# Kernel tuning notes

Measured on AMD Instinct MI355X. Metric: run time of the kernel, lower is better.

Reference implementation:

```python
import jax, jax.numpy as jnp
import numpy as np

D_MODEL = 512
D_STATE = 16
D_INNER = 2 * D_MODEL  # expand_factor=2
IN_CH = 256
B_SZ, H_SZ, W_SZ = 4, 32, 32


def setup_inputs() -> dict:
    key = jax.random.key(0)
    ks = jax.random.split(key, 24)
    f = jax.random.normal
    inp = {}
    inp["x_V"] = f(ks[0], (B_SZ, IN_CH, H_SZ, W_SZ), jnp.float32)
    inp["x_I"] = f(ks[1], (B_SZ, IN_CH, H_SZ, W_SZ), jnp.float32)
    # channel_reduce: 1x1 conv + BN (inference stats)
    inp["conv_red_w"] = f(ks[2], (D_MODEL, IN_CH), jnp.float32) * 0.05
    inp["bn_red_g"] = jnp.ones((D_MODEL,), jnp.float32)
    inp["bn_red_b"] = jnp.zeros((D_MODEL,), jnp.float32)
    inp["bn_red_m"] = jnp.zeros((D_MODEL,), jnp.float32)
    inp["bn_red_v"] = jnp.ones((D_MODEL,), jnp.float32)
    # channel_restore: 1x1 conv + BN
    inp["conv_res_w"] = f(ks[3], (IN_CH, D_MODEL), jnp.float32) * 0.05
    inp["bn_res_g"] = jnp.ones((IN_CH,), jnp.float32)
    inp["bn_res_b"] = jnp.zeros((IN_CH,), jnp.float32)
    inp["bn_res_m"] = jnp.zeros((IN_CH,), jnp.float32)
    inp["bn_res_v"] = jnp.ones((IN_CH,), jnp.float32)
    # lambda_predictor convs (1x1 on pooled features == linear)
    inp["lam_w1"] = f(ks[4], (D_MODEL // 4, D_MODEL * 2), jnp.float32) * 0.05
    inp["lam_b1"] = jnp.zeros((D_MODEL // 4,), jnp.float32)
    inp["lam_w2"] = f(ks[5], (2, D_MODEL // 4), jnp.float32) * 0.05
    inp["lam_b2"] = jnp.zeros((2,), jnp.float32)
    # two SimplifiedMamba2Blocks
    for i, p in enumerate(["V", "I"]):
        kk = jax.random.split(ks[6 + i], 6)
        inp[p + "_in_w"] = f(kk[0], (2 * D_INNER, D_MODEL), jnp.float32) * 0.03
        inp[p + "_out_w"] = f(kk[1], (D_MODEL, D_INNER), jnp.float32) * 0.03
        # A = -exp(A_log) in (-1, -0.05): stable decay
        inp[p + "_A_log"] = jnp.log(jax.random.uniform(kk[2], (D_INNER, D_STATE), jnp.float32, 0.05, 0.95))
        inp[p + "_B"] = f(kk[3], (D_INNER, D_STATE), jnp.float32) * 0.05
        inp[p + "_C"] = jnp.full((D_INNER, D_STATE), 0.01, jnp.float32)
        inp[p + "_ln_g"] = jnp.ones((D_MODEL,), jnp.float32)
        inp[p + "_ln_b"] = jnp.zeros((D_MODEL,), jnp.float32)
    inp["gate"] = jnp.asarray(0.1, jnp.float32)
    return inp


def _bn(x, g, b, m, v):
    # x: (B,C,H,W); inference-mode batchnorm
    return (x - m[:, None, None]) / jnp.sqrt(v[:, None, None] + 1e-5) * g[:, None, None] + b[:, None, None]


def _conv1x1(x, w):
    return jnp.einsum('bchw,oc->bohw', x, w)


def _ssm_scan(x_ssm, A, Bm, Cm, reverse):
    # x_ssm: (B,L,I); A,Bm,Cm: (I,S)
    bsz = x_ssm.shape[0]
    h0 = jnp.zeros((bsz, A.shape[0], A.shape[1]), x_ssm.dtype)

    def step(h, xt):  # xt: (B,I)
        h = jnp.clip(h * A + xt[:, :, None] * Bm, -10.0, 10.0)
        return h, jnp.einsum('bis,is->bi', h, Cm)

    _, ys = jax.lax.scan(step, h0, jnp.swapaxes(x_ssm, 0, 1), reverse=reverse)
    return jnp.swapaxes(ys, 0, 1)  # (B,L,I), in original time order


def _mamba(x, ln_g, ln_b, in_w, out_w, A_log, Bm, Cm):
    # LayerNorm
    mu = jnp.mean(x, -1, keepdims=True)
    var = jnp.mean((x - mu) ** 2, -1, keepdims=True)
    xn = (x - mu) / jnp.sqrt(var + 1e-5) * ln_g + ln_b
    xp = xn @ in_w.T  # (B,L,2*I)
    x_ssm, gate = jnp.split(xp, 2, axis=-1)
    A = jnp.clip(-jnp.exp(A_log), -10.0, -0.01)
    yf = _ssm_scan(x_ssm, A, Bm, Cm, False)
    yb = _ssm_scan(x_ssm, A, Bm, Cm, True)
    out = 0.5 * (yf + yb) * jax.nn.silu(gate)
    return out @ out_w.T


def reference(x_V, x_I, conv_red_w, bn_red_g, bn_red_b, bn_red_m, bn_red_v,
              conv_res_w, bn_res_g, bn_res_b, bn_res_m, bn_res_v,
              lam_w1, lam_b1, lam_w2, lam_b2,
              V_in_w, V_out_w, V_A_log, V_B, V_C, V_ln_g, V_ln_b,
              I_in_w, I_out_w, I_A_log, I_B, I_C, I_ln_g, I_ln_b, gate):
    B, _, H, W = x_V.shape
    xVr = jax.nn.relu(_bn(_conv1x1(x_V, conv_red_w), bn_red_g, bn_red_b, bn_red_m, bn_red_v))
    xIr = jax.nn.relu(_bn(_conv1x1(x_I, conv_red_w), bn_red_g, bn_red_b, bn_red_m, bn_red_v))
    # same spatial size -> adaptive pooling and [:B] slicing are identities
    conc = jnp.concatenate([xVr, xIr], axis=1)  # (B, 2*d_model, H, W)

    def lam(c):
        p = jnp.mean(c, axis=(2, 3))  # global avg pool -> (B, 2*d_model)
        h1 = jax.nn.relu(p @ lam_w1.T + lam_b1)
        return jax.nn.softmax(h1 @ lam_w2.T + lam_b2, axis=-1)  # (B,2)

    lamV = lam(conc)
    lamI = lam(conc)

    seq_V = jnp.swapaxes(xVr.reshape(B, D_MODEL, H * W), 1, 2)  # (B,L,D)
    seq_I = jnp.swapaxes(xIr.reshape(B, D_MODEL, H * W), 1, 2)

    outV_std = _mamba(seq_V, V_ln_g, V_ln_b, V_in_w, V_out_w, V_A_log, V_B, V_C)
    outI_std = _mamba(seq_I, I_ln_g, I_ln_b, I_in_w, I_out_w, I_A_log, I_B, I_C)
    outV_cross = _mamba(seq_V, V_ln_g, V_ln_b, V_in_w, V_out_w, V_A_log, jax.lax.stop_gradient(I_B), V_C)
    outI_cross = _mamba(seq_I, I_ln_g, I_ln_b, I_in_w, I_out_w, I_A_log, jax.lax.stop_gradient(V_B), I_C)

    outV = lamV[:, 0][:, None, None] * outV_std + lamV[:, 1][:, None, None] * outV_cross
    outI = lamI[:, 0][:, None, None] * outI_std + lamI[:, 1][:, None, None] * outI_cross

    featV = jnp.swapaxes(outV, 1, 2).reshape(B, D_MODEL, H, W)
    featI = jnp.swapaxes(outI, 1, 2).reshape(B, D_MODEL, H, W)
    featV = _bn(_conv1x1(featV, conv_res_w), bn_res_g, bn_res_b, bn_res_m, bn_res_v)
    featI = _bn(_conv1x1(featI, conv_res_w), bn_res_g, bn_res_b, bn_res_m, bn_res_v)

    g = jax.nn.sigmoid(gate)
    return (x_V + g * featV, x_I + g * featI)
```

## Files before the change

kernel.cpp:

```cpp
#include <hip/hip_runtime.h>
#include <hip/hip_bf16.h>
#include <math.h>

#define L_SZ 1024
#define DM   512
#define DI   1024
#define NS   16
#define CH   256

typedef float4 f4;
typedef __attribute__((ext_vector_type(8))) short short8;
typedef __attribute__((ext_vector_type(8))) unsigned short u16x8;
typedef __attribute__((ext_vector_type(4))) float f32x4;

__device__ __forceinline__ float bf2f(ushort u) {
    union { unsigned int i; float f; } x; x.i = ((unsigned int)u) << 16; return x.f;
}
__device__ __forceinline__ ushort f2bf(float f) {
    union { float f; unsigned int i; } x; x.f = f;
    unsigned int r = x.i + 0x7FFFu + ((x.i >> 16) & 1u);
    return (ushort)(r >> 16);
}
__device__ __forceinline__ uint pkbf(float a, float b) {
    union { __hip_bfloat162 h; uint u; } c;
    c.h = __float22bfloat162_rn(make_float2(a, b));
    return c.u;
}

#define GLOAD16(gp, lp) \
  __builtin_amdgcn_global_load_lds((const __attribute__((address_space(1))) void*)(gp), \
                                   (__attribute__((address_space(3))) void*)(lp), 16, 0, 0)

__global__ __launch_bounds__(256) void k_prep(
    const float* __restrict__ s0, const float* __restrict__ s1,
    const float* __restrict__ s2, const float* __restrict__ s3,
    const float* __restrict__ s4, const float* __restrict__ s5,
    ushort* __restrict__ d0, ushort* __restrict__ d1,
    ushort* __restrict__ d2, ushort* __restrict__ d3,
    ushort* __restrict__ d4, ushort* __restrict__ d5,
    const float* __restrict__ xv, const float* __restrict__ xi,
    ushort* __restrict__ xtv, ushort* __restrict__ xti,
    float* __restrict__ p, unsigned int* __restrict__ cnt)
{
    __shared__ float tile[32][36];
    const int bid = blockIdx.x;
    const int t = threadIdx.x;
    if (bid < 2304) {
        const float* s; ushort* d; int rel;
        if      (bid < 128)  { s = s0; d = d0; rel = bid; }
        else if (bid < 256)  { s = s1; d = d1; rel = bid - 128; }
        else if (bid < 1280) { s = s2; d = d2; rel = bid - 256; }
        else                 { s = s3; d = d3; rel = bid - 1280; }
        const int i = rel * 256 + t;
        f4 v = ((const f4*)s)[i];
        ushort4 o;
        o.x = f2bf(v.x); o.y = f2bf(v.y); o.z = f2bf(v.z); o.w = f2bf(v.w);
        ((ushort4*)d)[i] = o;
        return;
    }
    if (bid < 3328) {
        const int rel = (bid < 2816) ? bid - 2304 : bid - 2816;
        const float* wo = (bid < 2816) ? s4 : s5;
        ushort* wt      = (bid < 2816) ? d4 : d5;
        const int kt = rel & 31, dt = rel >> 5;
        const int d0_ = dt * 32, k0 = kt * 32;
        {
            int cc = t >> 3, ll4 = (t & 7) << 2;
            f4 v = *(const f4*)(wo + (size_t)(d0_ + cc) * 1024 + k0 + ll4);
            tile[cc][ll4 + 0] = v.x; tile[cc][ll4 + 1] = v.y;
            tile[cc][ll4 + 2] = v.z; tile[cc][ll4 + 3] = v.w;
        }
        __syncthreads();
        {
            int ll = t >> 3, cc4 = (t & 7) << 2;
            ushort4 o;
            o.x = f2bf(tile[cc4 + 0][ll]); o.y = f2bf(tile[cc4 + 1][ll]);
            o.z = f2bf(tile[cc4 + 2][ll]); o.w = f2bf(tile[cc4 + 3][ll]);
            *(ushort4*)(wt + (size_t)(k0 + ll) * 512 + d0_ + cc4) = o;
        }
        return;
    }
    if (bid < 5376) {
        const int rel = bid - 3328;
        const int l0 = (rel & 31) * 32, c0 = ((rel >> 5) & 7) * 32;
        const int z = rel >> 8;
        const int b = z & 3, st = z >> 2;
        const float* x = st ? xi : xv;
        ushort* xt = st ? xti : xtv;
        {
            int cc = t >> 3, ll4 = (t & 7) << 2;
            f4 v = *(const f4*)(x + ((size_t)(b * CH + c0 + cc)) * L_SZ + l0 + ll4);
            tile[cc][ll4 + 0] = v.x; tile[cc][ll4 + 1] = v.y;
            tile[cc][ll4 + 2] = v.z; tile[cc][ll4 + 3] = v.w;
        }
        __syncthreads();
        {
            int ll = t >> 3, cc4 = (t & 7) << 2;
            ushort4 o;
            o.x = f2bf(tile[cc4 + 0][ll]); o.y = f2bf(tile[cc4 + 1][ll]);
            o.z = f2bf(tile[cc4 + 2][ll]); o.w = f2bf(tile[cc4 + 3][ll]);
            *(ushort4*)(xt + ((size_t)(b * L_SZ + l0 + ll)) * CH + c0 + cc4) = o;
        }
        return;
    }
    const f4 z4 = {0.f, 0.f, 0.f, 0.f};
    ((f4*)p)[t]       = z4;
    ((f4*)p)[t + 256] = z4;
    ((f4*)p)[t + 512] = z4;
    ((f4*)p)[t + 768] = z4;
    if (t == 0) *cnt = 0u;
}

template<int MODE, int BM, int BN, int OS>
__global__ __launch_bounds__(256) void k_gemm(
    const ushort* __restrict__ A0, const ushort* __restrict__ A1,
    const ushort* __restrict__ B0, const ushort* __restrict__ B1,
    int K,
    float* __restrict__ o0, float* __restrict__ o1,
    ushort* __restrict__ ob0, ushort* __restrict__ ob1,
    ushort* __restrict__ sb0, ushort* __restrict__ sb1,
    const float* __restrict__ pg, const float* __restrict__ pb,
    const float* __restrict__ pm, const float* __restrict__ pv,
    const float* __restrict__ x0, const float* __restrict__ x1,
    const float* __restrict__ gate, float* __restrict__ pp)
{
    constexpr int MT   = BM / 32;
    constexpr int NT   = BN / 32;
    constexpr int ASEG = BM / 16;
    constexpr int NSEG = (BM + BN) / 16;
    constexpr int SPW  = NSEG / 4;
    __shared__ __align__(16) ushort Sl[2][(BM + BN) * 32];
    const int t = threadIdx.x;
    const int wv = t >> 6, lane = t & 63;
    const int n0 = blockIdx.x * BN, m0 = blockIdx.y * BM;
    const int st = blockIdx.z;
    const ushort* Ap = st ? A1 : A0;
    const ushort* Bp = st ? B1 : B0;
    const int wm = wv >> 1, wn = wv & 1;
    const int lrow = lane & 15, q = lane >> 4;
    f32x4 acc[MT][NT];
    #pragma unroll
    for (int a_ = 0; a_ < MT; ++a_)
        #pragma unroll
        for (int b_ = 0; b_ < NT; ++b_)
            acc[a_][b_] = (f32x4){0.f, 0.f, 0.f, 0.f};
    const int srow = lane >> 2;
    const int skk  = (((lane & 3) ^ ((lane >> 3) & 3)) << 3);
    const int koff = ((q ^ ((lrow >> 1) & 3)) << 3);
    #pragma unroll
    for (int s2 = 0; s2 < SPW; ++s2) {
        const int seg = wv * SPW + s2;
        const int grow = (seg < ASEG) ? (m0 + seg * 16 + srow)
                                      : (n0 + (seg - ASEG) * 16 + srow);
        const ushort* src = (seg < ASEG) ? Ap : Bp;
        GLOAD16(src + (size_t)grow * K + skk, &Sl[0][seg * 512]);
    }
    int cur = 0;
    for (int k0 = 0; k0 < K; k0 += 32) {
        if (k0 + 32 < K) {
            #pragma unroll
            for (int s2 = 0; s2 < SPW; ++s2) {
                const int seg = wv * SPW + s2;
                const int grow = (seg < ASEG) ? (m0 + seg * 16 + srow)
                                              : (n0 + (seg - ASEG) * 16 + srow);
                const ushort* src = (seg < ASEG) ? Ap : Bp;
                GLOAD16(src + (size_t)grow * K + (k0 + 32) + skk, &Sl[cur ^ 1][seg * 512]);
            }
            if constexpr (SPW == 2)      asm volatile("s_waitcnt vmcnt(2)" ::: "memory");
            else if constexpr (SPW == 3) asm volatile("s_waitcnt vmcnt(3)" ::: "memory");
            else                         asm volatile("s_waitcnt vmcnt(4)" ::: "memory");
        } else {
            asm volatile("s_waitcnt vmcnt(0)" ::: "memory");
        }
        __builtin_amdgcn_s_barrier();
        short8 af[MT], bfr[NT];
        #pragma unroll
        for (int mt = 0; mt < MT; ++mt)
            af[mt] = *(const short8*)&Sl[cur][(wm * (MT * 16) + mt * 16 + lrow) * 32 + koff];
        #pragma unroll
        for (int nt = 0; nt < NT; ++nt)
            bfr[nt] = *(const short8*)&Sl[cur][(BM + wn * (NT * 16) + nt * 16 + lrow) * 32 + koff];
        #pragma unroll
        for (int mt = 0; mt < MT; ++mt)
            #pragma unroll
            for (int nt = 0; nt < NT; ++nt) {
                if constexpr (MODE == 1)
                    acc[mt][nt] = __builtin_amdgcn_mfma_f32_16x16x32_bf16(bfr[nt], af[mt], acc[mt][nt], 0, 0, 0);
                else
                    acc[mt][nt] = __builtin_amdgcn_mfma_f32_16x16x32_bf16(af[mt], bfr[nt], acc[mt][nt], 0, 0, 0);
            }
        asm volatile("s_waitcnt lgkmcnt(0)" ::: "memory");
        __builtin_amdgcn_sched_barrier(0);
        __builtin_amdgcn_s_barrier();
        cur ^= 1;
    }
    if (MODE == 0) {
        ushort* sq = st ? ob1 : ob0;
        const int b = m0 >> 10;
        #pragma unroll
        for (int nt = 0; nt < NT; ++nt) {
            const int gn = n0 + wn * (NT * 16) + nt * 16 + lrow;
            const float s  = pg[gn] * rsqrtf(pv[gn] + 1e-5f);
            const float sh = pb[gn] - pm[gn] * s;
            float psum = 0.f;
            #pragma unroll
            for (int mt = 0; mt < MT; ++mt) {
                const int gm = m0 + wm * (MT * 16) + mt * 16 + q * 4;
                float v[4];
                #pragma unroll
                for (int r = 0; r < 4; ++r) {
                    v[r] = fmaxf(fmaf(acc[mt][nt][r], s, sh), 0.f);
                    psum += v[r];
                }
                const uint u01 = pkbf(v[0], v[1]);
                const uint u23 = pkbf(v[2], v[3]);
                ushort* bp = sq + (size_t)gm * DM + gn;
                bp[0]      = (ushort)u01;
                bp[DM]     = (ushort)(u01 >> 16);
                bp[2 * DM] = (ushort)u23;
                bp[3 * DM] = (ushort)(u23 >> 16);
            }
            psum += __shfl_xor(psum, 16, 64);
            psum += __shfl_xor(psum, 32, 64);
            if (q == 0)
                atomicAdd(pp + (b * 1024 + st * 512 + gn), psum * (1.0f / 1024.0f));
        }
    } else if (MODE == 1) {
        const bool isx = (n0 < 1024);
        ushort* xp = st ? ob1 : ob0;
        ushort* sp = st ? sb1 : sb0;
        #pragma unroll
        for (int mt = 0; mt < MT; ++mt) {
            const int gm = m0 + wm * (MT * 16) + mt * 16 + lrow;
            #pragma unroll
            for (int nt = 0; nt < NT; ++nt) {
                const int gnb = n0 + wn * (NT * 16) + nt * 16 + q * 4;
                if (isx) {
                    const uint u01 = pkbf(acc[mt][nt][0], acc[mt][nt][1]);
                    const uint u23 = pkbf(acc[mt][nt][2], acc[mt][nt][3]);
                    *(uint2*)(xp + (size_t)gm * DI + gnb) = make_uint2(u01, u23);
                } else {
                    float sv[4];
                    #pragma unroll
                    for (int r = 0; r < 4; ++r) {
                        const float v = acc[mt][nt][r];
                        sv[r] = v / (1.f + __expf(-v));
                    }
                    const uint u01 = pkbf(sv[0], sv[1]);
                    const uint u23 = pkbf(sv[2], sv[3]);
                    *(uint2*)(sp + (size_t)gm * DI + gnb - 1024) = make_uint2(u01, u23);
                }
            }
        }
    } else if (MODE == 2) {
        ushort* fp_ = st ? ob1 : ob0;
        #pragma unroll
        for (int nt = 0; nt < NT; ++nt) {
            const int gn = n0 + wn * (NT * 16) + nt * 16 + lrow;
            #pragma unroll
            for (int mt = 0; mt < MT; ++mt) {
                const int gm = m0 + wm * (MT * 16) + mt * 16 + q * 4;
                const uint u01 = pkbf(acc[mt][nt][0], acc[mt][nt][1]);
                const uint u23 = pkbf(acc[mt][nt][2], acc[mt][nt][3]);
                ushort* bp = fp_ + (size_t)gm * OS + gn;
                bp[0]      = (ushort)u01;
                bp[OS]     = (ushort)(u01 >> 16);
                bp[2 * OS] = (ushort)u23;
                bp[3 * OS] = (ushort)(u23 >> 16);
            }
        }
    } else {
        const float* xin = st ? x1 : x0;
        float* op = st ? o1 : o0;
        const float g = 1.f / (1.f + __expf(-gate[0]));
        #pragma unroll
        for (int nt = 0; nt < NT; ++nt) {
            const int gn = n0 + wn * (NT * 16) + nt * 16 + lrow;
            const float s  = pg[gn] * rsqrtf(pv[gn] + 1e-5f);
            const float sh = pb[gn] - pm[gn] * s;
            #pragma unroll
            for (int mt = 0; mt < MT; ++mt) {
                const int gmb = m0 + wm * (MT * 16) + mt * 16 + q * 4;
                const int b = gmb >> 10, l = gmb & 1023;
                const size_t off = ((size_t)(b * CH + gn)) * L_SZ + l;
                f4 xi = *(const f4*)(xin + off);
                f4 o;
                o.x = xi.x + g * fmaf(acc[mt][nt][0], s, sh);
                o.y = xi.y + g * fmaf(acc[mt][nt][1], s, sh);
                o.z = xi.z + g * fmaf(acc[mt][nt][2], s, sh);
                o.w = xi.w + g * fmaf(acc[mt][nt][3], s, sh);
                *(f4*)(op + off) = o;
            }
        }
    }
}

__global__ __launch_bounds__(256) void k_lnlam(
    const ushort* __restrict__ seq0, const ushort* __restrict__ seq1,
    const float* __restrict__ g0, const float* __restrict__ b0,
    const float* __restrict__ g1, const float* __restrict__ b1,
    ushort* __restrict__ ln0, ushort* __restrict__ ln1,
    const float* __restrict__ p, const float* __restrict__ w1,
    const float* __restrict__ lb1, const float* __restrict__ w2,
    const float* __restrict__ lb2, float* __restrict__ h1,
    float* __restrict__ lamo, unsigned int* __restrict__ cnt)
{
    const int t = threadIdx.x, lane = t & 63, wv = t >> 6;
    if (blockIdx.x >= 1024) {
        __shared__ float lsm[8];
        __shared__ unsigned int tick;
        const int lbk = (blockIdx.x - 1024) * 2 + blockIdx.y;
        const int idx = lbk * 4 + wv;
        const int b = idx >> 7, j = idx & 127;
        const float* pb = p + b * 1024;
        const float* wr = w1 + j * 1024;
        float s = 0.f;
        #pragma unroll
        for (int k = 0; k < 16; ++k)
            s = fmaf(pb[lane + k * 64], wr[lane + k * 64], s);
        #pragma unroll
        for (int off = 1; off < 64; off <<= 1) s += __shfl_xor(s, off, 64);
        if (lane == 0) h1[idx] = fmaxf(s + lb1[j], 0.f);
        __threadfence();
        __syncthreads();
        if (t == 0) tick = atomicAdd(cnt, 1u);
        __syncthreads();
        if (tick != 127u) return;
        __threadfence();
        {
            const int g32 = t >> 5, l32 = t & 31;
            const int bb = g32 >> 1, kk = g32 & 1;
            const float* hb = h1 + bb * 128;
            const float* wr2 = w2 + kk * 128;
            float ss = 0.f;
            #pragma unroll
            for (int u = 0; u < 4; ++u)
                ss = fmaf(hb[l32 + u * 32], wr2[l32 + u * 32], ss);
            #pragma unroll
            for (int off = 1; off < 32; off <<= 1) ss += __shfl_xor(ss, off, 64);
            if (l32 == 0) lsm[g32] = ss + lb2[kk];
        }
        __syncthreads();
        if (t < 4) {
            const float a0 = lsm[t * 2], a1 = lsm[t * 2 + 1];
            const float m  = fmaxf(a0, a1);
            const float e0 = __expf(a0 - m), e1 = __expf(a1 - m);
            const float inv = 1.f / (e0 + e1);
            lamo[t * 2 + 0] = e0 * inv;
            lamo[t * 2 + 1] = e1 * inv;
        }
        return;
    }
    const int row = blockIdx.x * 4 + wv, st = blockIdx.y;
    const ushort* seq = st ? seq1 : seq0;
    const float* gg  = st ? g1 : g0;
    const float* bb  = st ? b1 : b0;
    ushort* ln = st ? ln1 : ln0;
    const u16x8 v = *(const u16x8*)(seq + (size_t)row * DM + lane * 8);
    float f[8];
    float s = 0.f, ss = 0.f;
    #pragma unroll
    for (int i = 0; i < 8; ++i) {
        f[i] = bf2f(v[i]);
        s += f[i];
        ss = fmaf(f[i], f[i], ss);
    }
    #pragma unroll
    for (int off = 1; off < 64; off <<= 1) {
        s += __shfl_xor(s, off, 64); ss += __shfl_xor(ss, off, 64);
    }
    const float mu = s * (1.f / 512.f);
    const float rstd = rsqrtf(ss * (1.f / 512.f) - mu * mu + 1e-5f);
    const f4 gv0 = *(const f4*)(gg + lane * 8);
    const f4 gv1 = *(const f4*)(gg + lane * 8 + 4);
    const f4 bv0 = *(const f4*)(bb + lane * 8);
    const f4 bv1 = *(const f4*)(bb + lane * 8 + 4);
    const float gvv[8] = {gv0.x, gv0.y, gv0.z, gv0.w, gv1.x, gv1.y, gv1.z, gv1.w};
    const float bvv[8] = {bv0.x, bv0.y, bv0.z, bv0.w, bv1.x, bv1.y, bv1.z, bv1.w};
    u16x8 o;
    #pragma unroll
    for (int i = 0; i < 8; i += 2) {
        const uint u = pkbf(fmaf((f[i]     - mu) * rstd, gvv[i],     bvv[i]),
                            fmaf((f[i + 1] - mu) * rstd, gvv[i + 1], bvv[i + 1]));
        o[i]     = (ushort)u;
        o[i + 1] = (ushort)(u >> 16);
    }
    *(u16x8*)(ln + (size_t)row * DM + lane * 8) = o;
}

__global__ __launch_bounds__(128, 2) void k_scan(
    const ushort* __restrict__ xsV, const ushort* __restrict__ xsI,
    const ushort* __restrict__ sgV, const ushort* __restrict__ sgI,
    const float* __restrict__ VA, const float* __restrict__ VB,
    const float* __restrict__ VC, const float* __restrict__ IA,
    const float* __restrict__ IB, const float* __restrict__ IC,
    const float* __restrict__ lam,
    ushort* __restrict__ yV, ushort* __restrict__ yI)
{
    __shared__ __align__(16) ushort xt[256][64];
    const int t = threadIdx.x;
    const int dir = t & 1;
    const int il = t >> 1;
    const int b = blockIdx.y;
    const int st = blockIdx.z >> 3, j = blockIdx.z & 7;
    const int c0 = blockIdx.x * 64;
    const ushort* xrow  = (st ? xsI : xsV) + (size_t)b * L_SZ * DI + c0;
    const ushort* sgrow = (st ? sgI : sgV) + (size_t)b * L_SZ * DI + c0;
    ushort* yrow        = (st ? yI  : yV ) + (size_t)b * L_SZ * DI + c0;
    const float* Alog = st ? IA : VA;
    const float* Cm   = st ? IC : VC;
    const float* Bown = st ? IB : VB;
    const float* Both = st ? VB : IB;
    const float lam0 = lam[b * 2 + 0], lam1 = lam[b * 2 + 1];
    const int row0 = j << 7;
    const int srow = t >> 3;
    const int scol = (t & 7) << 3;
    #pragma unroll
    for (int i = 0; i < 16; ++i) {
        int r = row0 - 64 + i * 16 + srow;
        r = max(0, min(1023, r));
        GLOAD16(xrow + (size_t)r * DI + scol, &xt[i * 16 + srow][0]);
    }
    float a[16], w[16], g[16];
    {
        const int cb = (c0 + il) * NS;
        #pragma unroll
        for (int s4 = 0; s4 < 4; ++s4) {
            const f4 av = *(const f4*)(Alog + cb + s4 * 4);
            const f4 cv = *(const f4*)(Cm   + cb + s4 * 4);
            const f4 bo = *(const f4*)(Bown + cb + s4 * 4);
            const f4 bt = *(const f4*)(Both + cb + s4 * 4);
            const float avv[4] = {av.x, av.y, av.z, av.w};
            const float cvv[4] = {cv.x, cv.y, cv.z, cv.w};
            const float bov[4] = {bo.x, bo.y, bo.z, bo.w};
            const float btv[4] = {bt.x, bt.y, bt.z, bt.w};
            #pragma unroll
            for (int q = 0; q < 4; ++q) {
                const int s = s4 * 4 + q;
                a[s] = fminf(fmaxf(-__expf(avv[q]), -10.f), -0.01f);
                w[s] = 0.5f * cvv[q] * fmaf(lam0, bov[q], lam1 * btv[q]);
                g[s] = 0.f;
            }
        }
    }
    __syncthreads();

    const ushort* xtf = &xt[0][0];
    int toff = (dir ? 255 : 0) * 64 + il;
    const int tstep = dir ? -64 : 64;

    float vp0, vp1, vp2, vp3;

#define XPRE(V) { V = bf2f(xtf[toff]); toff += tstep; }
#define UPD(V) { _Pragma("unroll") \
    for (int s = 0; s < 16; ++s) g[s] = fmaf(a[s], g[s], V); }
#define YROW(V, Y) { float ye_ = 0.f, yo_ = 0.f; \
    _Pragma("unroll") \
    for (int s = 0; s < 8; ++s) { \
        g[s]     = fmaf(a[s],     g[s],     V); ye_ = fmaf(g[s],     w[s],     ye_); \
        g[s + 8] = fmaf(a[s + 8], g[s + 8], V); yo_ = fmaf(g[s + 8], w[s + 8], yo_); \
    } \
    Y = ye_ + yo_; }

    XPRE(vp0) XPRE(vp1) XPRE(vp2) XPRE(vp3)
    #pragma unroll
    for (int k = 0; k < 16; ++k) {
        UPD(vp0) XPRE(vp0) UPD(vp1) XPRE(vp1)
        UPD(vp2) XPRE(vp2) UPD(vp3) XPRE(vp3)
    }
    if ((j == 0 && dir == 0) || (j == 7 && dir == 1)) {
        #pragma unroll
        for (int s = 0; s < 16; ++s) g[s] = 0.f;
    }

#define SP4(WA, WB) { float y0_, y1_, y2_, y3_; \
    YROW(vp0, y0_) XPRE(vp0) YROW(vp1, y1_) XPRE(vp1) \
    YROW(vp2, y2_) XPRE(vp2) YROW(vp3, y3_) XPRE(vp3) \
    WA = (uint)f2bf(y0_) | ((uint)f2bf(y1_) << 16); \
    WB = (uint)f2bf(y2_) | ((uint)f2bf(y3_) << 16); }

#define SGPRE(K, S0, S1, S2, S3) { \
    S0 = bf2f(sgrow[(size_t)(row0 + (dir ? (63 - 2*(K))     : (64 + 2*(K))))     * DI + il]); \
    S1 = bf2f(sgrow[(size_t)(row0 + (dir ? (62 - 2*(K))     : (65 + 2*(K))))     * DI + il]); \
    S2 = bf2f(sgrow[(size_t)(row0 + (dir ? (61 - 2*(K))     : (66 + 2*(K))))     * DI + il]); \
    S3 = bf2f(sgrow[(size_t)(row0 + (dir ? (60 - 2*(K))     : (67 + 2*(K))))     * DI + il]); }

#define F4(K, W1, W2, S0, S1, S2, S3) { \
    const uint p1_ = __shfl_xor(W1, 1, 64); \
    float y_; \
    YROW(vp0, y_) XPRE(vp0) \
    { const int r_ = row0 + (dir ? (63 - 2*(K)) : (64 + 2*(K))); \
      yrow[(size_t)r_ * DI + il] = f2bf((y_ + bf2f((ushort)(p1_ >> 16))) * S0); } \
    YROW(vp1, y_) XPRE(vp1) \
    { const int r_ = row0 + (dir ? (62 - 2*(K)) : (65 + 2*(K))); \
      yrow[(size_t)r_ * DI + il] = f2bf((y_ + bf2f((ushort)(p1_ & 0xFFFFu))) * S1); } \
    const uint p2_ = __shfl_xor(W2, 1, 64); \
    YROW(vp2, y_) XPRE(vp2) \
    { const int r_ = row0 + (dir ? (61 - 2*(K)) : (66 + 2*(K))); \
      yrow[(size_t)r_ * DI + il] = f2bf((y_ + bf2f((ushort)(p2_ >> 16))) * S2); } \
    YROW(vp3, y_) XPRE(vp3) \
    { const int r_ = row0 + (dir ? (60 - 2*(K)) : (67 + 2*(K))); \
      yrow[(size_t)r_ * DI + il] = f2bf((y_ + bf2f((ushort)(p2_ & 0xFFFFu))) * S3); } }

    uint s00, s01, s02, s03, s04, s05, s06, s07;
    uint s08, s09, s10, s11, s12, s13, s14, s15;
    uint s16, s17, s18, s19, s20, s21, s22, s23;
    uint s24, s25, s26, s27, s28, s29, s30, s31;

    SP4(s00, s01) SP4(s02, s03) SP4(s04, s05) SP4(s06, s07)
    SP4(s08, s09) SP4(s10, s11) SP4(s12, s13) SP4(s14, s15)
    SP4(s16, s17) SP4(s18, s19) SP4(s20, s21) SP4(s22, s23)
    SP4(s24, s25) SP4(s26, s27) SP4(s28, s29) SP4(s30, s31)

    float sa0, sa1, sa2, sa3, sb0, sb1, sb2, sb3;
    SGPRE(0,  sa0, sa1, sa2, sa3)
    SGPRE(2,  sb0, sb1, sb2, sb3)
    F4(0,  s31, s30, sa0, sa1, sa2, sa3) SGPRE(4,  sa0, sa1, sa2, sa3)
    F4(2,  s29, s28, sb0, sb1, sb2, sb3) SGPRE(6,  sb0, sb1, sb2, sb3)
    F4(4,  s27, s26, sa0, sa1, sa2, sa3) SGPRE(8,  sa0, sa1, sa2, sa3)
    F4(6,  s25, s24, sb0, sb1, sb2, sb3) SGPRE(10, sb0, sb1, sb2, sb3)
    F4(8,  s23, s22, sa0, sa1, sa2, sa3) SGPRE(12, sa0, sa1, sa2, sa3)
    F4(10, s21, s20, sb0, sb1, sb2, sb3) SGPRE(14, sb0, sb1, sb2, sb3)
    F4(12, s19, s18, sa0, sa1, sa2, sa3) SGPRE(16, sa0, sa1, sa2, sa3)
    F4(14, s17, s16, sb0, sb1, sb2, sb3) SGPRE(18, sb0, sb1, sb2, sb3)
    F4(16, s15, s14, sa0, sa1, sa2, sa3) SGPRE(20, sa0, sa1, sa2, sa3)
    F4(18, s13, s12, sb0, sb1, sb2, sb3) SGPRE(22, sb0, sb1, sb2, sb3)
    F4(20, s11, s10, sa0, sa1, sa2, sa3) SGPRE(24, sa0, sa1, sa2, sa3)
    F4(22, s09, s08, sb0, sb1, sb2, sb3) SGPRE(26, sb0, sb1, sb2, sb3)
    F4(24, s07, s06, sa0, sa1, sa2, sa3) SGPRE(28, sa0, sa1, sa2, sa3)
    F4(26, s05, s04, sb0, sb1, sb2, sb3) SGPRE(30, sb0, sb1, sb2, sb3)
    F4(28, s03, s02, sa0, sa1, sa2, sa3)
    F4(30, s01, s00, sb0, sb1, sb2, sb3)

#undef XPRE
#undef UPD
#undef YROW
#undef SP4
#undef SGPRE
#undef F4
}

extern "C" void kernel_launch(void* const* d_in, const int* in_sizes, int n_in,
                              void* d_out, int out_size, void* d_ws, size_t ws_size,
                              hipStream_t stream)
{
    const float* xV       = (const float*)d_in[0];
    const float* xI       = (const float*)d_in[1];
    const float* convredw = (const float*)d_in[2];
    const float* bnredg   = (const float*)d_in[3];
    const float* bnredb   = (const float*)d_in[4];
    const float* bnredm   = (const float*)d_in[5];
    const float* bnredv   = (const float*)d_in[6];
    const float* convresw = (const float*)d_in[7];
    const float* bnresg   = (const float*)d_in[8];
    const float* bnresb   = (const float*)d_in[9];
    const float* bnresm   = (const float*)d_in[10];
    const float* bnresv   = (const float*)d_in[11];
    const float* lamw1    = (const float*)d_in[12];
    const float* lamb1    = (const float*)d_in[13];
    const float* lamw2    = (const float*)d_in[14];
    const float* lamb2    = (const float*)d_in[15];
    const float* Vinw     = (const float*)d_in[16];
    const float* Voutw    = (const float*)d_in[17];
    const float* VAlog    = (const float*)d_in[18];
    const float* VB       = (const float*)d_in[19];
    const float* VC       = (const float*)d_in[20];
    const float* Vlng     = (const float*)d_in[21];
    const float* Vlnb     = (const float*)d_in[22];
    const float* Iinw     = (const float*)d_in[23];
    const float* Ioutw    = (const float*)d_in[24];
    const float* IAlog    = (const float*)d_in[25];
    const float* IB       = (const float*)d_in[26];
    const float* IC       = (const float*)d_in[27];
    const float* Ilng     = (const float*)d_in[28];
    const float* Ilnb     = (const float*)d_in[29];
    const float* gate     = (const float*)d_in[30];

    char* W = (char*)d_ws;
    const size_t MB = 1048576;
    ushort* seqV  = (ushort*)(W + 0);
    ushort* seqI  = (ushort*)(W + 4  * MB);
    float*  p     = (float*)(W + 8 * MB);
    float*  lam   = (float*)(W + 8 * MB + 16384);
    float*  h1    = (float*)(W + 8 * MB + 32768);
    unsigned int* cnt = (unsigned int*)(W + 8 * MB + 49152);
    ushort* sgV   = (ushort*)(W + 17 * MB);
    ushort* sgI   = (ushort*)(W + 25 * MB);
    ushort* yV    = (ushort*)(W + 33 * MB);
    ushort* yI    = (ushort*)(W + 41 * MB);
    ushort* wred  = (ushort*)(W + 65 * MB);
    ushort* wres  = (ushort*)(W + 65 * MB + 262144);
    ushort* winV  = (ushort*)(W + 66 * MB);
    ushort* winI  = (ushort*)(W + 68 * MB);
    ushort* woTv  = (ushort*)(W + 70 * MB);
    ushort* woTi  = (ushort*)(W + 71 * MB);
    ushort* xtV   = (ushort*)(W + 72 * MB);
    ushort* xtI   = (ushort*)(W + 74 * MB);
    ushort* lnV   = (ushort*)(W + 76 * MB);
    ushort* lnI   = (ushort*)(W + 80 * MB);
    ushort* xsV   = (ushort*)(W + 84 * MB);
    ushort* xsI   = (ushort*)(W + 92 * MB);
    ushort* wcombV = (ushort*)(W + 100 * MB);
    ushort* wcombI = (ushort*)(W + 100 * MB + 524288);
    float*  outp  = (float*)d_out;

    k_prep<<<dim3(5377), 256, 0, stream>>>(
        convredw, convresw, Vinw, Iinw, Voutw, Ioutw,
        wred, wres, winV, winI, woTv, woTi,
        xV, xI, xtV, xtI, p, cnt);
    k_gemm<2, 64, 64, 1024><<<dim3(16, 4, 2), 256, 0, stream>>>(
        wres, wres, woTv, woTi, 512,
        nullptr, nullptr, wcombV, wcombI, nullptr, nullptr,
        nullptr, nullptr, nullptr, nullptr, nullptr, nullptr, nullptr, nullptr);
    k_gemm<0, 128, 64, 512><<<dim3(8, 32, 2), 256, 0, stream>>>(xtV, xtI, wred, wred, 256,
        nullptr, nullptr, seqV, seqI, nullptr, nullptr,
        bnredg, bnredb, bnredm, bnredv, nullptr, nullptr, nullptr, p);
    k_lnlam<<<dim3(1088, 2), 256, 0, stream>>>(
        seqV, seqI, Vlng, Vlnb, Ilng, Ilnb, lnV, lnI,
        p, lamw1, lamb1, lamw2, lamb2, h1, lam, cnt);
    k_gemm<1, 128, 128, 512><<<dim3(16, 32, 2), 256, 0, stream>>>(lnV, lnI, winV, winI, 512,
        nullptr, nullptr, xsV, xsI, sgV, sgI,
        nullptr, nullptr, nullptr, nullptr, nullptr, nullptr, nullptr, nullptr);
    k_scan<<<dim3(16, 4, 16), 128, 0, stream>>>(xsV, xsI, sgV, sgI,
        VAlog, VB, VC, IAlog, IB, IC, lam, yV, yI);
    k_gemm<3, 64, 64, 512><<<dim3(4, 64, 2), 256, 0, stream>>>(yV, yI, wcombV, wcombI, 1024,
        outp, outp + 1048576, nullptr, nullptr, nullptr, nullptr,
        bnresg, bnresb, bnresm, bnresv, xV, xI, gate, nullptr);
}
```

Before: 232.9 us.

## Split scan state across thread pairs and exchange directions via shared memory

Doubles the scan block to 256 threads. Each channel's 16-state recurrence is now split across two lanes of 8 states each, with a shuffle to combine partial outputs, and the two scan directions are placed in separate wavefront halves. The register-held packed-output scheme with shuffles between adjacent direction lanes is replaced by a shared-memory buffer that holds the first half of one direction's outputs, followed by a block barrier. This is meant to raise parallelism and cut the serial per-thread chain length and register pressure. In exchange it adds redundant recurrence updates, an extra shuffle per step, a barrier, and shared-memory traffic.

Result: slower. 272.2 us (+16.8%).

```diff
diff --git a/kernel.cpp b/kernel.cpp
--- a/kernel.cpp
+++ b/kernel.cpp
@@ -388,7 +388,7 @@
     *(u16x8*)(ln + (size_t)row * DM + lane * 8) = o;
 }
 
-__global__ __launch_bounds__(128, 2) void k_scan(
+__global__ __launch_bounds__(256, 2) void k_scan(
     const ushort* __restrict__ xsV, const ushort* __restrict__ xsI,
     const ushort* __restrict__ sgV, const ushort* __restrict__ sgI,
     const float* __restrict__ VA, const float* __restrict__ VB,
@@ -398,9 +398,11 @@
     ushort* __restrict__ yV, ushort* __restrict__ yI)
 {
     __shared__ __align__(16) ushort xt[256][64];
+    __shared__ ushort ys[2][64][64];
     const int t = threadIdx.x;
-    const int dir = t & 1;
-    const int il = t >> 1;
+    const int dir = t >> 7;
+    const int shalf = t & 1;
+    const int il = (t & 127) >> 1;
     const int b = blockIdx.y;
     const int st = blockIdx.z >> 3, j = blockIdx.z & 7;
     const int c0 = blockIdx.x * 64;
@@ -416,16 +418,16 @@
     const int srow = t >> 3;
     const int scol = (t & 7) << 3;
     #pragma unroll
-    for (int i = 0; i < 16; ++i) {
-        int r = row0 - 64 + i * 16 + srow;
+    for (int i = 0; i < 8; ++i) {
+        int r = row0 - 64 + i * 32 + srow;
         r = max(0, min(1023, r));
-        GLOAD16(xrow + (size_t)r * DI + scol, &xt[i * 16 + srow][0]);
-    }
-    float a[16], w[16], g[16];
+        GLOAD16(xrow + (size_t)r * DI + scol, &xt[i * 32 + srow][0]);
+    }
+    float a[8], w[8], g[8];
     {
-        const int cb = (c0 + il) * NS;
-        #pragma unroll
-        for (int s4 = 0; s4 < 4; ++s4) {
+        const int cb = (c0 + il) * NS + shalf * 8;
+        #pragma unroll
+        for (int s4 = 0; s4 < 2; ++s4) {
             const f4 av = *(const f4*)(Alog + cb + s4 * 4);
             const f4 cv = *(const f4*)(Cm   + cb + s4 * 4);
             const f4 bo = *(const f4*)(Bown + cb + s4 * 4);
@@ -449,95 +451,48 @@
     int toff = (dir ? 255 : 0) * 64 + il;
     const int tstep = dir ? -64 : 64;
 
-    float vp0, vp1, vp2, vp3;
-
-#define XPRE(V) { V = bf2f(xtf[toff]); toff += tstep; }
-#define UPD(V) { _Pragma("unroll") \
-    for (int s = 0; s < 16; ++s) g[s] = fmaf(a[s], g[s], V); }
-#define YROW(V, Y) { float ye_ = 0.f, yo_ = 0.f; \
-    _Pragma("unroll") \
-    for (int s = 0; s < 8; ++s) { \
-        g[s]     = fmaf(a[s],     g[s],     V); ye_ = fmaf(g[s],     w[s],     ye_); \
-        g[s + 8] = fmaf(a[s + 8], g[s + 8], V); yo_ = fmaf(g[s + 8], w[s + 8], yo_); \
-    } \
-    Y = ye_ + yo_; }
-
-    XPRE(vp0) XPRE(vp1) XPRE(vp2) XPRE(vp3)
-    #pragma unroll
-    for (int k = 0; k < 16; ++k) {
-        UPD(vp0) XPRE(vp0) UPD(vp1) XPRE(vp1)
-        UPD(vp2) XPRE(vp2) UPD(vp3) XPRE(vp3)
+    #pragma unroll 8
+    for (int n = 0; n < 64; ++n) {
+        const float v = bf2f(xtf[toff]); toff += tstep;
+        #pragma unroll
+        for (int s = 0; s < 8; ++s) g[s] = fmaf(a[s], g[s], v);
     }
     if ((j == 0 && dir == 0) || (j == 7 && dir == 1)) {
         #pragma unroll
-        for (int s = 0; s < 16; ++s) g[s] = 0.f;
-    }
-
-#define SP4(WA, WB) { float y0_, y1_, y2_, y3_; \
-    YROW(vp0, y0_) XPRE(vp0) YROW(vp1, y1_) XPRE(vp1) \
-    YROW(vp2, y2_) XPRE(vp2) YROW(vp3, y3_) XPRE(vp3) \
-    WA = (uint)f2bf(y0_) | ((uint)f2bf(y1_) << 16); \
-    WB = (uint)f2bf(y2_) | ((uint)f2bf(y3_) << 16); }
-
-#define SGPRE(K, S0, S1, S2, S3) { \
-    S0 = bf2f(sgrow[(size_t)(row0 + (dir ? (63 - 2*(K))     : (64 + 2*(K))))     * DI + il]); \
-    S1 = bf2f(sgrow[(size_t)(row0 + (dir ? (62 - 2*(K))     : (65 + 2*(K))))     * DI + il]); \
-    S2 = bf2f(sgrow[(size_t)(row0 + (dir ? (61 - 2*(K))     : (66 + 2*(K))))     * DI + il]); \
-    S3 = bf2f(sgrow[(size_t)(row0 + (dir ? (60 - 2*(K))     : (67 + 2*(K))))     * DI + il]); }
-
-#define F4(K, W1, W2, S0, S1, S2, S3) { \
-    const uint p1_ = __shfl_xor(W1, 1, 64); \
-    float y_; \
-    YROW(vp0, y_) XPRE(vp0) \
-    { const int r_ = row0 + (dir ? (63 - 2*(K)) : (64 + 2*(K))); \
-      yrow[(size_t)r_ * DI + il] = f2bf((y_ + bf2f((ushort)(p1_ >> 16))) * S0); } \
-    YROW(vp1, y_) XPRE(vp1) \
-    { const int r_ = row0 + (dir ? (62 - 2*(K)) : (65 + 2*(K))); \
-      yrow[(size_t)r_ * DI + il] = f2bf((y_ + bf2f((ushort)(p1_ & 0xFFFFu))) * S1); } \
-    const uint p2_ = __shfl_xor(W2, 1, 64); \
-    YROW(vp2, y_) XPRE(vp2) \
-    { const int r_ = row0 + (dir ? (61 - 2*(K)) : (66 + 2*(K))); \
-      yrow[(size_t)r_ * DI + il] = f2bf((y_ + bf2f((ushort)(p2_ >> 16))) * S2); } \
-    YROW(vp3, y_) XPRE(vp3) \
-    { const int r_ = row0 + (dir ? (60 - 2*(K)) : (67 + 2*(K))); \
-      yrow[(size_t)r_ * DI + il] = f2bf((y_ + bf2f((ushort)(p2_ & 0xFFFFu))) * S3); } }
-
-    uint s00, s01, s02, s03, s04, s05, s06, s07;
-    uint s08, s09, s10, s11, s12, s13, s14, s15;
-    uint s16, s17, s18, s19, s20, s21, s22, s23;
-    uint s24, s25, s26, s27, s28, s29, s30, s31;
-
-    SP4(s00, s01) SP4(s02, s03) SP4(s04, s05) SP4(s06, s07)
-    SP4(s08, s09) SP4(s10, s11) SP4(s12, s13) SP4(s14, s15)
-    SP4(s16, s17) SP4(s18, s19) SP4(s20, s21) SP4(s22, s23)
-    SP4(s24, s25) SP4(s26, s27) SP4(s28, s29) SP4(s30, s31)
-
-    float sa0, sa1, sa2, sa3, sb0, sb1, sb2, sb3;
-    SGPRE(0,  sa0, sa1, sa2, sa3)
-    SGPRE(2,  sb0, sb1, sb2, sb3)
-    F4(0,  s31, s30, sa0, sa1, sa2, sa3) SGPRE(4,  sa0, sa1, sa2, sa3)
-    F4(2,  s29, s28, sb0, sb1, sb2, sb3) SGPRE(6,  sb0, sb1, sb2, sb3)
-    F4(4,  s27, s26, sa0, sa1, sa2, sa3) SGPRE(8,  sa0, sa1, sa2, sa3)
-    F4(6,  s25, s24, sb0, sb1, sb2, sb3) SGPRE(10, sb0, sb1, sb2, sb3)
-    F4(8,  s23, s22, sa0, sa1, sa2, sa3) SGPRE(12, sa0, sa1, sa2, sa3)
-    F4(10, s21, s20, sb0, sb1, sb2, sb3) SGPRE(14, sb0, sb1, sb2, sb3)
-    F4(12, s19, s18, sa0, sa1, sa2, sa3) SGPRE(16, sa0, sa1, sa2, sa3)
-    F4(14, s17, s16, sb0, sb1, sb2, sb3) SGPRE(18, sb0, sb1, sb2, sb3)
-    F4(16, s15, s14, sa0, sa1, sa2, sa3) SGPRE(20, sa0, sa1, sa2, sa3)
-    F4(18, s13, s12, sb0, sb1, sb2, sb3) SGPRE(22, sb0, sb1, sb2, sb3)
-    F4(20, s11, s10, sa0, sa1, sa2, sa3) SGPRE(24, sa0, sa1, sa2, sa3)
-    F4(22, s09, s08, sb0, sb1, sb2, sb3) SGPRE(26, sb0, sb1, sb2, sb3)
-    F4(24, s07, s06, sa0, sa1, sa2, sa3) SGPRE(28, sa0, sa1, sa2, sa3)
-    F4(26, s05, s04, sb0, sb1, sb2, sb3) SGPRE(30, sb0, sb1, sb2, sb3)
-    F4(28, s03, s02, sa0, sa1, sa2, sa3)
-    F4(30, s01, s00, sb0, sb1, sb2, sb3)
-
-#undef XPRE
-#undef UPD
-#undef YROW
-#undef SP4
-#undef SGPRE
-#undef F4
+        for (int s = 0; s < 8; ++s) g[s] = 0.f;
+    }
+
+    #pragma unroll 8
+    for (int m = 0; m < 64; ++m) {
+        const float v = bf2f(xtf[toff]); toff += tstep;
+        float yh = 0.f;
+        #pragma unroll
+        for (int s = 0; s < 8; ++s) {
+            g[s] = fmaf(a[s], g[s], v);
+            yh   = fmaf(g[s], w[s], yh);
+        }
+        const float y = yh + __shfl_xor(yh, 1, 64);
+        if ((m & 1) == shalf) ys[dir][m][il] = f2bf(y);
+    }
+    __syncthreads();
+
+    #pragma unroll 8
+    for (int m = 64; m < 128; ++m) {
+        const float v = bf2f(xtf[toff]); toff += tstep;
+        float yh = 0.f;
+        #pragma unroll
+        for (int s = 0; s < 8; ++s) {
+            g[s] = fmaf(a[s], g[s], v);
+            yh   = fmaf(g[s], w[s], yh);
+        }
+        const float y = yh + __shfl_xor(yh, 1, 64);
+        if ((m & 1) == shalf) {
+            const int r = row0 + (dir ? 127 - m : m);
+            const float z = (y + bf2f(ys[dir ^ 1][127 - m][il]))
+                          * bf2f(sgrow[(size_t)r * DI + il]);
+            yrow[(size_t)r * DI + il] = f2bf(z);
+        }
+    }
 }
 
 extern "C" void kernel_launch(void* const* d_in, const int* in_sizes, int n_in,
@@ -621,7 +576,7 @@
     k_gemm<1, 128, 128, 512><<<dim3(16, 32, 2), 256, 0, stream>>>(lnV, lnI, winV, winI, 512,
         nullptr, nullptr, xsV, xsI, sgV, sgI,
         nullptr, nullptr, nullptr, nullptr, nullptr, nullptr, nullptr, nullptr);
-    k_scan<<<dim3(16, 4, 16), 128, 0, stream>>>(xsV, xsI, sgV, sgI,
+    k_scan<<<dim3(16, 4, 16), 256, 0, stream>>>(xsV, xsI, sgV, sgI,
         VAlog, VB, VC, IAlog, IB, IC, lam, yV, yI);
     k_gemm<3, 64, 64, 512><<<dim3(4, 64, 2), 256, 0, stream>>>(yV, yI, wcombV, wcombI, 1024,
         outp, outp + 1048576, nullptr, nullptr, nullptr, nullptr,
```
